# Kernel optimization log

Hardware: AMD Instinct MI355X
Metric: run time of the kernel (lower is better)

Reference implementation:

```python
import jax, jax.numpy as jnp
import numpy as np

BITS = 4
SIGNED_MIN, SIGNED_MAX = -(2 ** (BITS - 1)), 2 ** (BITS - 1) - 1      # int4: [-8, 7]
UNSIGNED_MIN, UNSIGNED_MAX = 0, 2 ** BITS - 1                          # uint4: [0, 15]
INT32_MIN, INT32_MAX = -(2.0 ** 31), 2.0 ** 31 - 1


def fake_quant(x, scale, qmin, qmax):
    """Brevitas-style fake quantization with straight-through rounding."""
    q = jnp.clip(jnp.round(x / scale), qmin, qmax) * scale
    # STE: identity gradient through round/clip
    return x + jax.lax.stop_gradient(q - x)


def weight_scale(W):
    # Brevitas default weight quantizer: per-tensor scale from max-abs stats
    return jax.lax.stop_gradient(jnp.max(jnp.abs(W))) / SIGNED_MAX


def setup_inputs() -> dict:
    key = jax.random.key(0)
    ks = jax.random.split(key, 5)
    B, S, D, F = 4, 2048, 2048, 8192
    return {
        "x": jax.random.normal(ks[0], (B, S, D), dtype=jnp.float32),
        "W1": jax.random.normal(ks[1], (F, D), dtype=jnp.float32) * 0.02,
        "b1": jax.random.normal(ks[2], (F,), dtype=jnp.float32) * 0.02,
        "W2": jax.random.normal(ks[3], (D, F), dtype=jnp.float32) * 0.02,
        "b2": jax.random.normal(ks[4], (D,), dtype=jnp.float32) * 0.02,
        "s_act1": jnp.full((1,), 0.1, dtype=jnp.float32),
        "s_act2": jnp.full((1,), 0.1, dtype=jnp.float32),
    }


def reference(x, W1, b1, W2, b2, s_act1, s_act2):
    s1 = s_act1[0]
    s2 = s_act2[0]

    # quantizer_1: signed int4 QuantIdentity on input
    x_q = fake_quant(x, s1, SIGNED_MIN, SIGNED_MAX)

    # w_1: int4 weight QuantLinear with Int32Bias (bias scale = in_scale * w_scale)
    sw1 = weight_scale(W1)
    W1_q = fake_quant(W1, sw1, SIGNED_MIN, SIGNED_MAX)
    b1_q = fake_quant(b1, s1 * sw1, INT32_MIN, INT32_MAX)
    h = jnp.einsum("bsd,fd->bsf", x_q, W1_q) + b1_q  # [B, S, d_ff]

    # quantizer_2: QuantReLU -> unsigned int4 fake-quant of relu(h)
    h_q = fake_quant(jax.nn.relu(h), s2, UNSIGNED_MIN, UNSIGNED_MAX)
    # dropout: identity in eval mode

    # w_2: int4 weight QuantLinear, input scale = s2
    sw2 = weight_scale(W2)
    W2_q = fake_quant(W2, sw2, SIGNED_MIN, SIGNED_MAX)
    b2_q = fake_quant(b2, s2 * sw2, INT32_MIN, INT32_MAX)
    out = jnp.einsum("bsf,df->bsd", h_q, W2_q) + b2_q  # [B, S, d_model]
    return out
```

## Files before the change

### kernel.cpp

```cpp
#include <hip/hip_runtime.h>

typedef int int32x4 __attribute__((ext_vector_type(4)));

__global__ void maxabs_kernel(const float* __restrict__ x, int n4,
                              unsigned* __restrict__ out) {
    float m = 0.f;
    int i = blockIdx.x * blockDim.x + threadIdx.x;
    int stride = gridDim.x * blockDim.x;
    const float4* x4 = (const float4*)x;
    for (int j = i; j < n4; j += stride) {
        float4 v = x4[j];
        m = fmaxf(m, fmaxf(fmaxf(fabsf(v.x), fabsf(v.y)),
                           fmaxf(fabsf(v.z), fabsf(v.w))));
    }
#pragma unroll
    for (int off = 32; off; off >>= 1)
        m = fmaxf(m, __shfl_down(m, off, 64));
    __shared__ float wm[4];
    int ln = threadIdx.x & 63, wv = threadIdx.x >> 6;
    if (ln == 0) wm[wv] = m;
    __syncthreads();
    if (threadIdx.x == 0) {
        float bm = fmaxf(fmaxf(wm[0], wm[1]), fmaxf(wm[2], wm[3]));
        atomicMax(out, __float_as_uint(bm));
    }
}

__global__ void quant_blocked_kernel(const float* __restrict__ src, int n4,
                                     int K, int kshift,
                                     const float* __restrict__ sptr, float sdiv,
                                     float lo, float hi, int* __restrict__ out) {
    float s = sptr[0] / sdiv;
    int i0 = blockIdx.x * blockDim.x + threadIdx.x;
    int stride = gridDim.x * blockDim.x;
    for (int o = i0; o < n4; o += stride) {
        int blk = o >> 12;
        int i = o & 4095;
        int row = i >> 5;
        int c = (i >> 2) & 7;
        int b4 = i & 3;
        int rowblk = blk >> kshift;
        int kblk = blk & ((1 << kshift) - 1);
        int co = c ^ (row & 7);
        long srcoff = (long)(rowblk * 128 + row) * K + (kblk << 7) + (co << 4) + (b4 << 2);
        float4 v = *(const float4*)(src + srcoff);
        int a = (int)fminf(fmaxf(rintf(v.x / s), lo), hi);
        int b = (int)fminf(fmaxf(rintf(v.y / s), lo), hi);
        int cc = (int)fminf(fmaxf(rintf(v.z / s), lo), hi);
        int d = (int)fminf(fmaxf(rintf(v.w / s), lo), hi);
        out[o] = (a & 255) | ((b & 255) << 8) | ((cc & 255) << 16) | ((d & 255) << 24);
    }
}

template <bool FIRST>
__global__ __launch_bounds__(256, 5)
void gemm_i8_kernel(const char* __restrict__ A, const char* __restrict__ B,
                    int N, int nkt,
                    const float* __restrict__ sa_ptr,
                    const float* __restrict__ wmax_ptr,
                    const float* __restrict__ bias,
                    const float* __restrict__ s2_ptr,
                    char* __restrict__ out8, float* __restrict__ outf) {
    __shared__ __align__(16) char lA[128 * 128];
    __shared__ __align__(16) char lB[128 * 128];

    const int tid = threadIdx.x;
    const int wv = tid >> 6, ln = tid & 63;
    const int lnlo = ln & 15, lnhi = ln >> 4;
    const int wr = wv >> 1, wc = wv & 1;

    int32x4 acc[4][4] = {};

    const char* pa = A + ((size_t)blockIdx.y * nkt << 14);
    const char* pb = B + ((size_t)blockIdx.x * nkt << 14);

    for (int kt = 0; kt < nkt; ++kt) {
#pragma unroll
        for (int r = 0; r < 4; ++r) {
            int off = (r * 256 + tid) * 16;
            int lbase = (r * 256 + wv * 64) * 16;
            __builtin_amdgcn_global_load_lds(
                (const __attribute__((address_space(1))) void*)(pa + off),
                (__attribute__((address_space(3))) void*)(lA + lbase), 16, 0, 0);
            __builtin_amdgcn_global_load_lds(
                (const __attribute__((address_space(1))) void*)(pb + off),
                (__attribute__((address_space(3))) void*)(lB + lbase), 16, 0, 0);
        }
        pa += 16384;
        pb += 16384;
        __syncthreads();

        int32x4 af[4][2], bf[4][2];
#pragma unroll
        for (int mf = 0; mf < 4; ++mf)
#pragma unroll
            for (int kk = 0; kk < 2; ++kk) {
                int row = wr * 64 + mf * 16 + lnlo;
                int ch = kk * 4 + lnhi;
                af[mf][kk] = *(const int32x4*)(lA + row * 128 + ((ch ^ (row & 7)) * 16));
            }
#pragma unroll
        for (int nf = 0; nf < 4; ++nf)
#pragma unroll
            for (int kk = 0; kk < 2; ++kk) {
                int col = wc * 64 + nf * 16 + lnlo;
                int ch = kk * 4 + lnhi;
                bf[nf][kk] = *(const int32x4*)(lB + col * 128 + ((ch ^ (col & 7)) * 16));
            }

#pragma unroll
        for (int kk = 0; kk < 2; ++kk)
#pragma unroll
            for (int mf = 0; mf < 4; ++mf)
#pragma unroll
                for (int nf = 0; nf < 4; ++nf)
                    acc[mf][nf] = __builtin_amdgcn_mfma_i32_16x16x64_i8(
                        af[mf][kk], bf[nf][kk], acc[mf][nf], 0, 0, 0);
        __syncthreads();
    }

    float sa = sa_ptr[0];
    float sw = wmax_ptr[0] / 7.0f;
    float sab = sa * sw;
    float s2v = FIRST ? s2_ptr[0] : 0.f;

    char* hblk = FIRST ? out8 + (((size_t)blockIdx.y * gridDim.x + blockIdx.x) << 14)
                       : nullptr;

#pragma unroll
    for (int nf = 0; nf < 4; ++nf) {
        int lc = wc * 64 + nf * 16 + lnlo;
        long col = (long)blockIdx.x * 128 + lc;
        float bq = rintf(bias[col] / sab) * sab;
#pragma unroll
        for (int mf = 0; mf < 4; ++mf) {
            int lr0 = wr * 64 + mf * 16 + (lnhi << 2);
#pragma unroll
            for (int i = 0; i < 4; ++i) {
                int lr = lr0 + i;
                float h = sab * (float)acc[mf][nf][i] + bq;
                if constexpr (FIRST) {
                    h = fmaxf(h, 0.f);
                    float qv = fminf(fmaxf(rintf(h / s2v), 0.f), 15.f);
                    hblk[lr * 128 + (((lc >> 4) ^ (lr & 7)) << 4) + (lc & 15)] =
                        (char)(int)qv;
                } else {
                    outf[((long)blockIdx.y * 128 + lr) * N + col] = h;
                }
            }
        }
    }
}

extern "C" void kernel_launch(void* const* d_in, const int* in_sizes, int n_in,
                              void* d_out, int out_size, void* d_ws, size_t ws_size,
                              hipStream_t stream) {
    const float* x  = (const float*)d_in[0];
    const float* W1 = (const float*)d_in[1];
    const float* b1 = (const float*)d_in[2];
    const float* W2 = (const float*)d_in[3];
    const float* b2 = (const float*)d_in[4];
    const float* s1 = (const float*)d_in[5];
    const float* s2 = (const float*)d_in[6];

    const int M = 8192, D = 2048, F = 8192;

    char* ws = (char*)d_ws;
    unsigned* mx1 = (unsigned*)ws;
    unsigned* mx2 = (unsigned*)(ws + 4);
    char* xq  = ws + 256;
    char* w1q = xq + (size_t)M * D;
    char* w2q = w1q + (size_t)F * D;
    char* hq  = w2q + (size_t)D * F;

    hipMemsetAsync(d_ws, 0, 8, stream);

    maxabs_kernel<<<2048, 256, 0, stream>>>(W1, (F * D) >> 2, mx1);
    maxabs_kernel<<<2048, 256, 0, stream>>>(W2, (D * F) >> 2, mx2);

    quant_blocked_kernel<<<2048, 256, 0, stream>>>(
        x,  (M * D) >> 2, D, 4, s1, 1.f, -8.f, 7.f, (int*)xq);
    quant_blocked_kernel<<<2048, 256, 0, stream>>>(
        W1, (F * D) >> 2, D, 4, (const float*)mx1, 7.f, -8.f, 7.f, (int*)w1q);
    quant_blocked_kernel<<<2048, 256, 0, stream>>>(
        W2, (D * F) >> 2, F, 6, (const float*)mx2, 7.f, -8.f, 7.f, (int*)w2q);

    gemm_i8_kernel<true><<<dim3(F / 128, M / 128), 256, 0, stream>>>(
        xq, w1q, F, D / 128, s1, (const float*)mx1, b1, s2, hq, nullptr);

    gemm_i8_kernel<false><<<dim3(D / 128, M / 128), 256, 0, stream>>>(
        hq, w2q, D, F / 128, s2, (const float*)mx2, b2, nullptr, nullptr,
        (float*)d_out);
}
```

Measured before the change: 383.2 us.

## Halve GEMM K-tile to 64 with paired-row swizzled LDS layout

Shrinks the int8 GEMM K-tile from 128 to 64 bytes, so each block stages 16 KB of LDS instead of 32 KB. Two 64-byte rows are packed into each 128-byte LDS line with an XOR swizzle. The quantize kernels and the h output layout are changed to match this new blocked format. The likely aim is higher occupancy from the smaller LDS footprint, at the cost of twice as many K iterations and barriers, and only 16 MFMAs between each pair of syncs. Launch bounds are lowered from 5 to 4 waves.

```diff
diff --git a/kernel.cpp b/kernel.cpp
--- a/kernel.cpp
+++ b/kernel.cpp
@@ -34,26 +34,28 @@
     int i0 = blockIdx.x * blockDim.x + threadIdx.x;
     int stride = gridDim.x * blockDim.x;
     for (int o = i0; o < n4; o += stride) {
-        int blk = o >> 12;
-        int i = o & 4095;
-        int row = i >> 5;
-        int c = (i >> 2) & 7;
-        int b4 = i & 3;
+        int blk = o >> 11;
+        int i = o & 2047;
+        int v = i >> 5;
+        int sc = (i >> 2) & 7;
+        int w = i & 3;
+        int vc = sc ^ (v & 7);
+        int row = (v << 1) | (vc >> 2);
+        int chunk = vc & 3;
         int rowblk = blk >> kshift;
         int kblk = blk & ((1 << kshift) - 1);
-        int co = c ^ (row & 7);
-        long srcoff = (long)(rowblk * 128 + row) * K + (kblk << 7) + (co << 4) + (b4 << 2);
-        float4 v = *(const float4*)(src + srcoff);
-        int a = (int)fminf(fmaxf(rintf(v.x / s), lo), hi);
-        int b = (int)fminf(fmaxf(rintf(v.y / s), lo), hi);
-        int cc = (int)fminf(fmaxf(rintf(v.z / s), lo), hi);
-        int d = (int)fminf(fmaxf(rintf(v.w / s), lo), hi);
-        out[o] = (a & 255) | ((b & 255) << 8) | ((cc & 255) << 16) | ((d & 255) << 24);
+        long srcoff = (long)(rowblk * 128 + row) * K + (kblk << 6) + (chunk << 4) + (w << 2);
+        float4 f = *(const float4*)(src + srcoff);
+        int a = (int)fminf(fmaxf(rintf(f.x / s), lo), hi);
+        int b = (int)fminf(fmaxf(rintf(f.y / s), lo), hi);
+        int c = (int)fminf(fmaxf(rintf(f.z / s), lo), hi);
+        int d = (int)fminf(fmaxf(rintf(f.w / s), lo), hi);
+        out[o] = (a & 255) | ((b & 255) << 8) | ((c & 255) << 16) | ((d & 255) << 24);
     }
 }
 
 template <bool FIRST>
-__global__ __launch_bounds__(256, 5)
+__global__ __launch_bounds__(256, 4)
 void gemm_i8_kernel(const char* __restrict__ A, const char* __restrict__ B,
                     int N, int nkt,
                     const float* __restrict__ sa_ptr,
@@ -61,8 +63,8 @@
                     const float* __restrict__ bias,
                     const float* __restrict__ s2_ptr,
                     char* __restrict__ out8, float* __restrict__ outf) {
-    __shared__ __align__(16) char lA[128 * 128];
-    __shared__ __align__(16) char lB[128 * 128];
+    __shared__ __align__(16) char lA[128 * 64];
+    __shared__ __align__(16) char lB[128 * 64];
 
     const int tid = threadIdx.x;
     const int wv = tid >> 6, ln = tid & 63;
@@ -71,12 +73,12 @@
 
     int32x4 acc[4][4] = {};
 
-    const char* pa = A + ((size_t)blockIdx.y * nkt << 14);
-    const char* pb = B + ((size_t)blockIdx.x * nkt << 14);
+    const char* pa = A + ((size_t)blockIdx.y * nkt << 13);
+    const char* pb = B + ((size_t)blockIdx.x * nkt << 13);
 
     for (int kt = 0; kt < nkt; ++kt) {
 #pragma unroll
-        for (int r = 0; r < 4; ++r) {
+        for (int r = 0; r < 2; ++r) {
             int off = (r * 256 + tid) * 16;
             int lbase = (r * 256 + wv * 64) * 16;
             __builtin_amdgcn_global_load_lds(
@@ -86,36 +88,32 @@
                 (const __attribute__((address_space(1))) void*)(pb + off),
                 (__attribute__((address_space(3))) void*)(lB + lbase), 16, 0, 0);
         }
-        pa += 16384;
-        pb += 16384;
+        pa += 8192;
+        pb += 8192;
         __syncthreads();
 
-        int32x4 af[4][2], bf[4][2];
+        int32x4 af[4], bf[4];
+#pragma unroll
+        for (int mf = 0; mf < 4; ++mf) {
+            int row = wr * 64 + mf * 16 + lnlo;
+            int v = row >> 1;
+            int vc = ((row & 1) << 2) | lnhi;
+            af[mf] = *(const int32x4*)(lA + v * 128 + ((vc ^ (v & 7)) << 4));
+        }
+#pragma unroll
+        for (int nf = 0; nf < 4; ++nf) {
+            int col = wc * 64 + nf * 16 + lnlo;
+            int v = col >> 1;
+            int vc = ((col & 1) << 2) | lnhi;
+            bf[nf] = *(const int32x4*)(lB + v * 128 + ((vc ^ (v & 7)) << 4));
+        }
+
 #pragma unroll
         for (int mf = 0; mf < 4; ++mf)
 #pragma unroll
-            for (int kk = 0; kk < 2; ++kk) {
-                int row = wr * 64 + mf * 16 + lnlo;
-                int ch = kk * 4 + lnhi;
-                af[mf][kk] = *(const int32x4*)(lA + row * 128 + ((ch ^ (row & 7)) * 16));
-            }
-#pragma unroll
-        for (int nf = 0; nf < 4; ++nf)
-#pragma unroll
-            for (int kk = 0; kk < 2; ++kk) {
-                int col = wc * 64 + nf * 16 + lnlo;
-                int ch = kk * 4 + lnhi;
-                bf[nf][kk] = *(const int32x4*)(lB + col * 128 + ((ch ^ (col & 7)) * 16));
-            }
-
-#pragma unroll
-        for (int kk = 0; kk < 2; ++kk)
-#pragma unroll
-            for (int mf = 0; mf < 4; ++mf)
-#pragma unroll
-                for (int nf = 0; nf < 4; ++nf)
-                    acc[mf][nf] = __builtin_amdgcn_mfma_i32_16x16x64_i8(
-                        af[mf][kk], bf[nf][kk], acc[mf][nf], 0, 0, 0);
+            for (int nf = 0; nf < 4; ++nf)
+                acc[mf][nf] = __builtin_amdgcn_mfma_i32_16x16x64_i8(
+                    af[mf], bf[nf], acc[mf][nf], 0, 0, 0);
         __syncthreads();
     }
 
@@ -123,9 +121,6 @@
     float sw = wmax_ptr[0] / 7.0f;
     float sab = sa * sw;
     float s2v = FIRST ? s2_ptr[0] : 0.f;
-
-    char* hblk = FIRST ? out8 + (((size_t)blockIdx.y * gridDim.x + blockIdx.x) << 14)
-                       : nullptr;
 
 #pragma unroll
     for (int nf = 0; nf < 4; ++nf) {
@@ -142,7 +137,13 @@
                 if constexpr (FIRST) {
                     h = fmaxf(h, 0.f);
                     float qv = fminf(fmaxf(rintf(h / s2v), 0.f), 15.f);
-                    hblk[lr * 128 + (((lc >> 4) ^ (lr & 7)) << 4) + (lc & 15)] =
+                    int kblk = (blockIdx.x << 1) | (lc >> 6);
+                    int l6 = lc & 63;
+                    int v = lr >> 1;
+                    int vc = ((lr & 1) << 2) | (l6 >> 4);
+                    size_t blkoff =
+                        ((size_t)blockIdx.y * (gridDim.x << 1) + kblk) << 13;
+                    out8[blkoff + v * 128 + ((vc ^ (v & 7)) << 4) + (lc & 15)] =
                         (char)(int)qv;
                 } else {
                     outf[((long)blockIdx.y * 128 + lr) * N + col] = h;
@@ -179,16 +180,16 @@
     maxabs_kernel<<<2048, 256, 0, stream>>>(W2, (D * F) >> 2, mx2);
 
     quant_blocked_kernel<<<2048, 256, 0, stream>>>(
-        x,  (M * D) >> 2, D, 4, s1, 1.f, -8.f, 7.f, (int*)xq);
+        x,  (M * D) >> 2, D, 5, s1, 1.f, -8.f, 7.f, (int*)xq);
     quant_blocked_kernel<<<2048, 256, 0, stream>>>(
-        W1, (F * D) >> 2, D, 4, (const float*)mx1, 7.f, -8.f, 7.f, (int*)w1q);
+        W1, (F * D) >> 2, D, 5, (const float*)mx1, 7.f, -8.f, 7.f, (int*)w1q);
     quant_blocked_kernel<<<2048, 256, 0, stream>>>(
-        W2, (D * F) >> 2, F, 6, (const float*)mx2, 7.f, -8.f, 7.f, (int*)w2q);
+        W2, (D * F) >> 2, F, 7, (const float*)mx2, 7.f, -8.f, 7.f, (int*)w2q);
 
     gemm_i8_kernel<true><<<dim3(F / 128, M / 128), 256, 0, stream>>>(
-        xq, w1q, F, D / 128, s1, (const float*)mx1, b1, s2, hq, nullptr);
+        xq, w1q, F, D / 64, s1, (const float*)mx1, b1, s2, hq, nullptr);
 
     gemm_i8_kernel<false><<<dim3(D / 128, M / 128), 256, 0, stream>>>(
-        hq, w2q, D, F / 128, s2, (const float*)mx2, b2, nullptr, nullptr,
+        hq, w2q, D, F / 64, s2, (const float*)mx2, b2, nullptr, nullptr,
         (float*)d_out);
 }
```

Result: faster. 375.4 us (-2.0%).
